# Performance work log

Measured on AMD Instinct MI355X. Metric: run time of the kernel, lower is better.

Reference implementation:

```python
import jax, jax.numpy as jnp
import numpy as np

LAMBDA_VOLUME = 0.2
LAMBDA_WEIGHTED_ADJ = 0.15
LAMBDA_SYM = 0.05
AGE_MAX = 100.0
EPS_ROW = 1e-8
EPS_STD = 1e-6


def _smooth_l1(x):
    # F.smooth_l1_loss(x, 0) with beta=1, mean reduction
    ax = jnp.abs(x)
    return jnp.mean(jnp.where(ax < 1.0, 0.5 * x * x, ax - 0.5))


def setup_inputs() -> dict:
    key = jax.random.key(0)
    ks = jax.random.split(key, 9)
    B, C, X = 2, 32, 96
    logits = jax.random.normal(ks[0], (B, C, X, X, X), dtype=jnp.float32)
    age = jax.random.uniform(ks[1], (B, 1), dtype=jnp.float32) * AGE_MAX
    w_young = jax.random.uniform(ks[2], (C, C), dtype=jnp.float32)
    w_old = jax.random.uniform(ks[3], (C, C), dtype=jnp.float32)
    # expected per-class volumes ~ total_voxels / C in scale
    vol_means_young = jax.random.uniform(ks[4], (C,), dtype=jnp.float32) * 50000.0
    vol_means_old = jax.random.uniform(ks[5], (C,), dtype=jnp.float32) * 50000.0
    vol_stds_young = jax.random.uniform(ks[6], (C,), dtype=jnp.float32) * 5000.0 + 1000.0
    vol_stds_old = jax.random.uniform(ks[7], (C,), dtype=jnp.float32) * 5000.0 + 1000.0
    prior_adj = jax.random.uniform(ks[8], (C, C), dtype=jnp.float32)
    # left-right pair permutation: class i <-> i + C//2
    perm = jnp.concatenate([jnp.arange(C // 2, C), jnp.arange(0, C // 2)]).astype(jnp.int64)
    return {"logits": logits, "age": age, "w_young": w_young, "w_old": w_old,
            "vol_means_young": vol_means_young, "vol_means_old": vol_means_old,
            "vol_stds_young": vol_stds_young, "vol_stds_old": vol_stds_old,
            "prior_adj": prior_adj, "perm": perm}


def reference(logits, age, w_young, w_old, vol_means_young, vol_means_old,
              vol_stds_young, vol_stds_old, prior_adj, perm):
    B, C = logits.shape[0], logits.shape[1]
    probs = jax.nn.softmax(logits, axis=1)  # (B,C,X,Y,Z)
    alpha = jnp.clip(age / AGE_MAX, 0.0, 1.0)  # (B,1) interpolation between age anchors

    # ---- weighted adjacency loss (temperature == 1.0 -> no pow) ----
    pf = probs.reshape(B, C, -1)                     # (B,C,N)
    A = jnp.einsum('bcn,bdn->bcd', pf, pf)           # bmm(probs, probs^T)
    A = A * (1.0 - jnp.eye(C, dtype=A.dtype))        # zero diagonal
    W = (1.0 - alpha)[:, :, None] * w_young[None] + alpha[:, :, None] * w_old[None]  # (B,C,C)
    A = A * W
    Aw = A.mean(axis=0)
    Aw = Aw / jnp.clip(Aw.sum(axis=1, keepdims=True), EPS_ROW)
    prior = prior_adj * (1.0 - jnp.eye(C, dtype=prior_adj.dtype))
    prior = prior / jnp.clip(prior.sum(axis=1, keepdims=True), EPS_ROW)
    loss_adj = jnp.mean(jnp.abs(Aw - prior))

    # ---- volume consistency loss ----
    pred_vol = probs.sum(axis=(2, 3, 4))             # (B,C)
    means = (1.0 - alpha) * vol_means_young[None] + alpha * vol_means_old[None]
    stds = (1.0 - alpha) * vol_stds_young[None] + alpha * vol_stds_old[None]
    loss_vol = _smooth_l1((pred_vol - means) / (stds + EPS_STD))

    # ---- symmetry consistency loss (flip along X axis = dim 2, swap LR pairs) ----
    p_flip = jnp.flip(probs, axis=2)
    p_swap = p_flip[:, perm]                         # channel permutation = pairwise swap
    loss_sym = jnp.mean(jnp.abs(probs - p_swap))

    total = (LAMBDA_WEIGHTED_ADJ * loss_adj
             + LAMBDA_VOLUME * loss_vol
             + LAMBDA_SYM * loss_sym)
    return total
```

## Files before the change

### kernel.cpp

```cpp
#include <hip/hip_runtime.h>
#include <math.h>

#define CX 32
#define XX 9216
#define X3 884736
#define CHUNKS_PER_B 13824
#define WAVES_PER_B 2048
#define NBLOCKS 1024
#define RSU 17
#define RS16 34
#define SLICE_W 1088

typedef short s8v __attribute__((ext_vector_type(8)));
typedef float f32x16 __attribute__((ext_vector_type(16)));

__device__ __forceinline__ unsigned bf16rne(float f) {
    unsigned u = __float_as_uint(f);
    return (u + (0x7fffu + ((u >> 16) & 1u))) >> 16;
}


__global__ __launch_bounds__(256, 4)
void main_pass(const float* __restrict__ logits,
               float* __restrict__ A_acc,
               float* __restrict__ sym_acc)
{
    __shared__ __align__(16) unsigned lds_u[8704];
    const int tid = threadIdx.x;
    const int w   = tid >> 6;
    const int l   = tid & 63;
    const int wid = blockIdx.x * 4 + w;
    const int b   = wid >> 11;
    const int wb  = wid & 2047;
    const int lane31 = l & 31;
    const int h = l >> 5;

    unsigned* const buf0 = lds_u + w * (2 * SLICE_W);
    const float* lg = logits + (size_t)b * (size_t)(CX * X3);

    f32x16 acc = {};
    float sym = 0.f;

    for (int it = 0, cg = wb; cg < CHUNKS_PER_B; ++it, cg += WAVES_PER_B) {
        unsigned* const sb = buf0 + (it & 1) * SLICE_W;
        int x   = cg / 288;
        int rem = (cg - x * 288) * 32 + lane31;
        int xx  = h ? (95 - x) : x;
        const float* gp = lg + (size_t)xx * XX + (size_t)rem;

        float p[CX];
#pragma unroll
        for (int c = 0; c < CX; ++c) p[c] = gp[(size_t)c * X3];
        float m = p[0];
#pragma unroll
        for (int c = 1; c < CX; ++c) m = fmaxf(m, p[c]);
        float ssum = 0.f;
#pragma unroll
        for (int c = 0; c < CX; ++c) { p[c] = __expf(p[c] - m); ssum += p[c]; }
        float inv = 1.f / ssum;
#pragma unroll
        for (int c = 0; c < CX; ++c) p[c] *= inv;

        unsigned* myrow = sb + l * RSU;
#pragma unroll
        for (int c2 = 0; c2 < 16; ++c2)
            myrow[c2] = bf16rne(p[2 * c2]) | (bf16rne(p[2 * c2 + 1]) << 16);

        __syncthreads();

        const unsigned* prow = sb + (l ^ 32) * RSU;
#pragma unroll
        for (int j = 0; j < 16; ++j) {
            unsigned q = prow[(j + 8) & 15];
            sym += fabsf(p[2 * j]     - __uint_as_float(q << 16));
            sym += fabsf(p[2 * j + 1] - __uint_as_float(q & 0xffff0000u));
        }

        const unsigned short* sb16 = (const unsigned short*)sb;
#pragma unroll
        for (int t = 0; t < 4; ++t) {
            s8v af;
#pragma unroll
            for (int j = 0; j < 8; ++j)
                af[j] = (short)sb16[(16 * t + 8 * h + j) * RS16 + lane31];
            acc = __builtin_amdgcn_mfma_f32_32x32x16_bf16(af, af, acc, 0, 0, 0);
        }
    }

    __syncthreads();
    float* lds_f = (float*)lds_u;
#pragma unroll
    for (int r = 0; r < 16; ++r) {
        int row = (r & 3) + 8 * (r >> 2) + 4 * h;
        lds_f[w * 1056 + row * 32 + lane31] = acc[r];
    }
    float sv = sym;
#pragma unroll
    for (int o = 32; o >= 1; o >>= 1) sv += __shfl_down(sv, o);
    if (l == 0) lds_f[4224 + w] = sv;
    __syncthreads();

    {
        float4 s = make_float4(0.f, 0.f, 0.f, 0.f);
#pragma unroll
        for (int ww = 0; ww < 4; ++ww) {
            const float4 v = *((const float4*)lds_f + ww * 264 + tid);
            s.x += v.x; s.y += v.y; s.z += v.z; s.w += v.w;
        }
        float* Ab = A_acc + b * (CX * CX) + tid * 4;
        atomicAdd(&Ab[0], s.x);
        atomicAdd(&Ab[1], s.y);
        atomicAdd(&Ab[2], s.z);
        atomicAdd(&Ab[3], s.w);
    }
    if (tid == 0)
        atomicAdd(sym_acc, lds_f[4224] + lds_f[4225] + lds_f[4226] + lds_f[4227]);
}

__global__ void finalize(const float* __restrict__ A_acc,
                         const float* __restrict__ sym,
                         const float* __restrict__ age,
                         const float* __restrict__ wy,  const float* __restrict__ wo,
                         const float* __restrict__ vmy, const float* __restrict__ vmo,
                         const float* __restrict__ vsy, const float* __restrict__ vso,
                         const float* __restrict__ prior,
                         float* __restrict__ out)
{
    const int t = threadIdx.x;
    float a0 = fminf(fmaxf(age[0] * 0.01f, 0.f), 1.f);
    float a1 = fminf(fmaxf(age[1] * 0.01f, 0.f), 1.f);

    const int bb = t >> 5, c = t & 31;
    float full = 0.f;
#pragma unroll
    for (int d = 0; d < CX; ++d) full += A_acc[bb * 1024 + c * CX + d];

    float part_vol;
    {
        float al = bb ? a1 : a0;
        float mean = (1.f - al) * vmy[c] + al * vmo[c];
        float sd   = (1.f - al) * vsy[c] + al * vso[c] + 1e-6f;
        float r  = (full - mean) / sd;
        float ar = fabsf(r);
        part_vol = (ar < 1.f) ? 0.5f * r * r : (ar - 0.5f);
    }

    float part_adj = 0.f;
    if (t < 32) {
        float awrow[CX], prow[CX];
        float rs = 0.f, ps = 0.f;
#pragma unroll
        for (int d = 0; d < CX; ++d) {
            float v = 0.f, pv = 0.f;
            if (d != c) {
                float A0v = A_acc[c * CX + d];
                float A1v = A_acc[1024 + c * CX + d];
                float w0 = (1.f - a0) * wy[c * CX + d] + a0 * wo[c * CX + d];
                float w1 = (1.f - a1) * wy[c * CX + d] + a1 * wo[c * CX + d];
                v  = 0.5f * (A0v * w0 + A1v * w1);
                pv = prior[c * CX + d];
            }
            awrow[d] = v;  rs += v;
            prow[d]  = pv; ps += pv;
        }
        rs = fmaxf(rs, 1e-8f);
        ps = fmaxf(ps, 1e-8f);
#pragma unroll
        for (int d = 0; d < CX; ++d)
            part_adj += fabsf(awrow[d] / rs - prow[d] / ps);
    }

#pragma unroll
    for (int off = 32; off >= 1; off >>= 1) {
        part_adj += __shfl_down(part_adj, off);
        part_vol += __shfl_down(part_vol, off);
    }
    if (t == 0) {
        float loss_adj = part_adj * (1.f / 1024.f);
        float loss_vol = part_vol * (1.f / 64.f);
        float loss_sym = sym[0] / 56623104.f;
        out[0] = 0.15f * loss_adj + 0.2f * loss_vol + 0.05f * loss_sym;
    }
}

extern "C" void kernel_launch(void* const* d_in, const int* in_sizes, int n_in,
                              void* d_out, int out_size, void* d_ws, size_t ws_size,
                              hipStream_t stream) {
    const float* logits = (const float*)d_in[0];
    const float* age    = (const float*)d_in[1];
    const float* wy     = (const float*)d_in[2];
    const float* wo     = (const float*)d_in[3];
    const float* vmy    = (const float*)d_in[4];
    const float* vmo    = (const float*)d_in[5];
    const float* vsy    = (const float*)d_in[6];
    const float* vso    = (const float*)d_in[7];
    const float* prior  = (const float*)d_in[8];

    float* ws    = (float*)d_ws;
    float* A_acc = ws;
    float* sym   = ws + 2048;

    hipMemsetAsync(d_ws, 0, 2049 * sizeof(float), stream);
    main_pass<<<NBLOCKS, 256, 0, stream>>>(logits, A_acc, sym);
    finalize<<<1, 64, 0, stream>>>(A_acc, sym, age, wy, wo,
                                   vmy, vmo, vsy, vso, prior, (float*)d_out);
}
```

Baseline: 391.3 us.

## Software-pipeline logit loads across chunks and drop per-iteration block barrier

Restructures the per-wave loop so the 32 channel loads for the next chunk are issued before processing the current chunk, using two register sets in ping-pong. The block-wide __syncthreads is replaced by an LDS wait only, since each wave reads just its own LDS slice. This aims to hide global memory latency and remove inter-wave barrier stalls, at the cost of doubled register pressure for the prefetched values, which may reduce occupancy under the launch bounds.

```diff
diff --git a/kernel.cpp b/kernel.cpp
--- a/kernel.cpp
+++ b/kernel.cpp
@@ -41,16 +41,21 @@
     f32x16 acc = {};
     float sym = 0.f;
 
-    for (int it = 0, cg = wb; cg < CHUNKS_PER_B; ++it, cg += WAVES_PER_B) {
-        unsigned* const sb = buf0 + (it & 1) * SLICE_W;
+    float pA[CX], pB[CX];
+
+    auto chunk_ptr = [&](int cg) -> const float* {
         int x   = cg / 288;
         int rem = (cg - x * 288) * 32 + lane31;
         int xx  = h ? (95 - x) : x;
-        const float* gp = lg + (size_t)xx * XX + (size_t)rem;
-
-        float p[CX];
+        return lg + (size_t)xx * XX + (size_t)rem;
+    };
+
+    auto load32 = [&](float* p, const float* gp) {
 #pragma unroll
         for (int c = 0; c < CX; ++c) p[c] = gp[(size_t)c * X3];
+    };
+
+    auto body = [&](float* p, unsigned* sb) {
         float m = p[0];
 #pragma unroll
         for (int c = 1; c < CX; ++c) m = fmaxf(m, p[c]);
@@ -66,7 +71,9 @@
         for (int c2 = 0; c2 < 16; ++c2)
             myrow[c2] = bf16rne(p[2 * c2]) | (bf16rne(p[2 * c2 + 1]) << 16);
 
-        __syncthreads();
+        __builtin_amdgcn_sched_barrier(0);
+        asm volatile("s_waitcnt lgkmcnt(0)" ::: "memory");
+        __builtin_amdgcn_sched_barrier(0);
 
         const unsigned* prow = sb + (l ^ 32) * RSU;
 #pragma unroll
@@ -85,6 +92,23 @@
                 af[j] = (short)sb16[(16 * t + 8 * h + j) * RS16 + lane31];
             acc = __builtin_amdgcn_mfma_f32_32x32x16_bf16(af, af, acc, 0, 0, 0);
         }
+    };
+
+    int cg = wb;
+    load32(pA, chunk_ptr(cg));
+    while (true) {
+        int cg1 = cg + WAVES_PER_B;
+        bool more1 = (cg1 < CHUNKS_PER_B);
+        if (more1) load32(pB, chunk_ptr(cg1));
+        body(pA, buf0);
+        if (!more1) break;
+
+        int cg2 = cg1 + WAVES_PER_B;
+        bool more2 = (cg2 < CHUNKS_PER_B);
+        if (more2) load32(pA, chunk_ptr(cg2));
+        body(pB, buf0 + SLICE_W);
+        if (!more2) break;
+        cg = cg2;
     }
 
     __syncthreads();
```

After: 375.5 us. 1.04x faster.

## Double-buffer logits into LDS via async global_load_lds with swizzled bf16 tile

Applied to the files above, without the earlier changes.

Replaces direct per-thread register loads of the 32 channels with asynchronous global-to-LDS 16-byte loads into two staging buffers, so the next chunk's fetch overlaps the current chunk's softmax and MFMA. Blocks shrink to two waves, each wave handles a contiguous set of chunks, and __syncthreads is replaced with waitcnt-based intra-wave sync. The bf16 tile uses an XOR-swizzled layout so the MFMA operand is a single 16-byte vector read, and the max and sum reductions are tree-structured. It lowers the wave count per block and relies on manual vmcnt accounting, which could break if the compiler reorders loads.

```diff
diff --git a/kernel.cpp b/kernel.cpp
--- a/kernel.cpp
+++ b/kernel.cpp
@@ -5,11 +5,8 @@
 #define XX 9216
 #define X3 884736
 #define CHUNKS_PER_B 13824
-#define WAVES_PER_B 2048
 #define NBLOCKS 1024
-#define RSU 17
-#define RS16 34
-#define SLICE_W 1088
+#define WPB 1024
 
 typedef short s8v __attribute__((ext_vector_type(8)));
 typedef float f32x16 __attribute__((ext_vector_type(16)));
@@ -19,102 +16,146 @@
     return (u + (0x7fffu + ((u >> 16) & 1u))) >> 16;
 }
 
-
-__global__ __launch_bounds__(256, 4)
+__device__ __forceinline__ void gload_lds16(const float* g, float* l) {
+    __builtin_amdgcn_global_load_lds(
+        (const __attribute__((address_space(1))) void*)g,
+        (__attribute__((address_space(3))) void*)l, 16, 0, 0);
+}
+
+
+__global__ __launch_bounds__(128, 2)
 void main_pass(const float* __restrict__ logits,
                float* __restrict__ A_acc,
                float* __restrict__ sym_acc)
 {
-    __shared__ __align__(16) unsigned lds_u[8704];
+    __shared__ __align__(16) float lds_f[10240];
     const int tid = threadIdx.x;
     const int w   = tid >> 6;
     const int l   = tid & 63;
-    const int wid = blockIdx.x * 4 + w;
-    const int b   = wid >> 11;
-    const int wb  = wid & 2047;
+    const int wid = blockIdx.x * 2 + w;
+    const int b   = wid >> 10;
+    const int wb  = wid & 1023;
     const int lane31 = l & 31;
     const int h = l >> 5;
 
-    unsigned* const buf0 = lds_u + w * (2 * SLICE_W);
+    float* const stA = lds_f + w * 4096;
+    float* const stB = stA + 2048;
+    unsigned char* const sbB = (unsigned char*)(lds_f + 8192 + w * 1024);
     const float* lg = logits + (size_t)b * (size_t)(CX * X3);
+
+    const int ci0   = l >> 4;
+    const int pos   = (l & 15) * 4;
+    const int posm  = pos & 31;
+    const int phalf = pos >> 5;
+
+    const int trips = (wb < 512) ? 14 : 13;
 
     f32x16 acc = {};
     float sym = 0.f;
-
-    for (int it = 0, cg = wb; cg < CHUNKS_PER_B; ++it, cg += WAVES_PER_B) {
-        unsigned* const sb = buf0 + (it & 1) * SLICE_W;
-        int x   = cg / 288;
-        int rem = (cg - x * 288) * 32 + lane31;
-        int xx  = h ? (95 - x) : x;
-        const float* gp = lg + (size_t)xx * XX + (size_t)rem;
-
-        float p[CX];
-#pragma unroll
-        for (int c = 0; c < CX; ++c) p[c] = gp[(size_t)c * X3];
-        float m = p[0];
-#pragma unroll
-        for (int c = 1; c < CX; ++c) m = fmaxf(m, p[c]);
-        float ssum = 0.f;
-#pragma unroll
-        for (int c = 0; c < CX; ++c) { p[c] = __expf(p[c] - m); ssum += p[c]; }
-        float inv = 1.f / ssum;
+    float p[CX];
+
+    auto stage = [&](float* buf, int cg) {
+        int x  = cg / 288;
+        int rb = (cg - x * 288) * 32;
+        int xx = phalf ? (95 - x) : x;
+        const float* gp = lg + (size_t)ci0 * X3 + (size_t)xx * XX + (rb + posm);
+#pragma unroll
+        for (int i = 0; i < 8; ++i)
+            gload_lds16(gp + (size_t)i * (size_t)(4 * X3), buf + i * 256);
+    };
+
+    stage(stA, wb);
+    for (int it = 0; it < trips; ++it) {
+        float* cur = (it & 1) ? stB : stA;
+        float* nxt = (it & 1) ? stA : stB;
+        if (it + 1 < trips) {
+            stage(nxt, wb + (it + 1) * WPB);
+            __builtin_amdgcn_sched_barrier(0);
+            asm volatile("s_waitcnt vmcnt(8)" ::: "memory");
+            __builtin_amdgcn_sched_barrier(0);
+        } else {
+            __builtin_amdgcn_sched_barrier(0);
+            asm volatile("s_waitcnt vmcnt(0)" ::: "memory");
+            __builtin_amdgcn_sched_barrier(0);
+        }
+
+#pragma unroll
+        for (int c = 0; c < CX; ++c) p[c] = cur[c * 64 + l];
+        float mx[16];
+#pragma unroll
+        for (int c = 0; c < 16; ++c) mx[c] = fmaxf(p[c], p[c + 16]);
+#pragma unroll
+        for (int s = 8; s >= 1; s >>= 1)
+#pragma unroll
+            for (int c = 0; c < s; ++c) mx[c] = fmaxf(mx[c], mx[c + s]);
+        float m = mx[0];
+        float s0 = 0.f, s1 = 0.f, s2 = 0.f, s3 = 0.f;
+#pragma unroll
+        for (int c = 0; c < CX; c += 4) {
+            p[c]     = __expf(p[c]     - m);
+            p[c + 1] = __expf(p[c + 1] - m);
+            p[c + 2] = __expf(p[c + 2] - m);
+            p[c + 3] = __expf(p[c + 3] - m);
+            s0 += p[c]; s1 += p[c + 1]; s2 += p[c + 2]; s3 += p[c + 3];
+        }
+        float inv = 1.f / ((s0 + s1) + (s2 + s3));
 #pragma unroll
         for (int c = 0; c < CX; ++c) p[c] *= inv;
 
-        unsigned* myrow = sb + l * RSU;
-#pragma unroll
-        for (int c2 = 0; c2 < 16; ++c2)
-            myrow[c2] = bf16rne(p[2 * c2]) | (bf16rne(p[2 * c2 + 1]) << 16);
-
-        __syncthreads();
-
-        const unsigned* prow = sb + (l ^ 32) * RSU;
-#pragma unroll
-        for (int j = 0; j < 16; ++j) {
-            unsigned q = prow[(j + 8) & 15];
-            sym += fabsf(p[2 * j]     - __uint_as_float(q << 16));
-            sym += fabsf(p[2 * j + 1] - __uint_as_float(q & 0xffff0000u));
-        }
-
-        const unsigned short* sb16 = (const unsigned short*)sb;
+#pragma unroll
+        for (int c = 0; c < CX; ++c) {
+            int byte = c * 128 + ((2 * l) ^ ((c & 7) << 4));
+            *(unsigned short*)(sbB + byte) = (unsigned short)bf16rne(p[c]);
+        }
+
+        __builtin_amdgcn_sched_barrier(0);
+        asm volatile("s_waitcnt lgkmcnt(0)" ::: "memory");
+        __builtin_amdgcn_sched_barrier(0);
+
+#pragma unroll
+        for (int c = 0; c < CX; ++c) {
+            int cc = (c + 16) & 31;
+            int byte = cc * 128 + ((2 * (l ^ 32)) ^ ((cc & 7) << 4));
+            unsigned q = *(const unsigned short*)(sbB + byte);
+            sym += fabsf(p[c] - __uint_as_float(q << 16));
+        }
+
 #pragma unroll
         for (int t = 0; t < 4; ++t) {
-            s8v af;
-#pragma unroll
-            for (int j = 0; j < 8; ++j)
-                af[j] = (short)sb16[(16 * t + 8 * h + j) * RS16 + lane31];
+            int byte = lane31 * 128 + ((32 * t + 16 * h) ^ ((lane31 & 7) << 4));
+            s8v af = *(const s8v*)(sbB + byte);
             acc = __builtin_amdgcn_mfma_f32_32x32x16_bf16(af, af, acc, 0, 0, 0);
         }
     }
 
     __syncthreads();
-    float* lds_f = (float*)lds_u;
 #pragma unroll
     for (int r = 0; r < 16; ++r) {
         int row = (r & 3) + 8 * (r >> 2) + 4 * h;
-        lds_f[w * 1056 + row * 32 + lane31] = acc[r];
+        lds_f[w * 1024 + row * 32 + lane31] = acc[r];
     }
     float sv = sym;
 #pragma unroll
     for (int o = 32; o >= 1; o >>= 1) sv += __shfl_down(sv, o);
-    if (l == 0) lds_f[4224 + w] = sv;
+    if (l == 0) lds_f[2048 + w] = sv;
     __syncthreads();
 
     {
-        float4 s = make_float4(0.f, 0.f, 0.f, 0.f);
-#pragma unroll
-        for (int ww = 0; ww < 4; ++ww) {
-            const float4 v = *((const float4*)lds_f + ww * 264 + tid);
-            s.x += v.x; s.y += v.y; s.z += v.z; s.w += v.w;
-        }
-        float* Ab = A_acc + b * (CX * CX) + tid * 4;
-        atomicAdd(&Ab[0], s.x);
-        atomicAdd(&Ab[1], s.y);
-        atomicAdd(&Ab[2], s.z);
-        atomicAdd(&Ab[3], s.w);
+        const float4* f4 = (const float4*)lds_f;
+        float4 u0 = f4[2 * tid],     v0 = f4[2 * tid + 256];
+        float4 u1 = f4[2 * tid + 1], v1 = f4[2 * tid + 257];
+        float* Ab = A_acc + b * (CX * CX) + tid * 8;
+        atomicAdd(&Ab[0], u0.x + v0.x);
+        atomicAdd(&Ab[1], u0.y + v0.y);
+        atomicAdd(&Ab[2], u0.z + v0.z);
+        atomicAdd(&Ab[3], u0.w + v0.w);
+        atomicAdd(&Ab[4], u1.x + v1.x);
+        atomicAdd(&Ab[5], u1.y + v1.y);
+        atomicAdd(&Ab[6], u1.z + v1.z);
+        atomicAdd(&Ab[7], u1.w + v1.w);
     }
     if (tid == 0)
-        atomicAdd(sym_acc, lds_f[4224] + lds_f[4225] + lds_f[4226] + lds_f[4227]);
+        atomicAdd(sym_acc, lds_f[2048] + lds_f[2049]);
 }
 
 __global__ void finalize(const float* __restrict__ A_acc,
@@ -201,7 +242,7 @@
     float* sym   = ws + 2048;
 
     hipMemsetAsync(d_ws, 0, 2049 * sizeof(float), stream);
-    main_pass<<<NBLOCKS, 256, 0, stream>>>(logits, A_acc, sym);
+    main_pass<<<NBLOCKS, 128, 0, stream>>>(logits, A_acc, sym);
     finalize<<<1, 64, 0, stream>>>(A_acc, sym, age, wy, wo,
                                    vmy, vmo, vsy, vso, prior, (float*)d_out);
 }
```

Measured after the change: 436.1 us. 1.11x slower.
